# Optimization experiments

Measured on AMD Instinct MI355X. Metric: run time of the kernel, lower is better.

Reference implementation:

```python
import jax, jax.numpy as jnp
import numpy as np


def _l2n(v, axis):
    # torch F.normalize: x / max(||x||, eps)
    return v / jnp.maximum(jnp.linalg.norm(v, axis=axis, keepdims=True), 1e-12)


def setup_inputs() -> dict:
    key = jax.random.key(0)
    ks = jax.random.split(key, 10)
    B, C, H, W = 32, 1536, 32, 32
    m, l, g, hid = 64, 128, 256, 512
    s = 0.02
    f32 = jnp.float32
    return {
        "x": jax.random.normal(ks[0], (B, C, H, W), f32),
        "t": jax.random.normal(ks[1], (B, C), f32),
        "Wc1": jax.random.normal(ks[2], (hid, C), f32) * s, "bc1": jnp.zeros(hid, f32),
        "Wc2": jax.random.normal(ks[3], (l, hid), f32) * s, "bc2": jnp.zeros(l, f32),
        "Ws1": jax.random.normal(ks[4], (hid, C), f32) * s, "bs1": jnp.zeros(hid, f32),
        "Ws2": jax.random.normal(ks[5], (m, hid), f32) * s, "bs2": jnp.zeros(m, f32),
        "Wt1": jax.random.normal(ks[6], (hid, C), f32) * s, "bt1": jnp.zeros(hid, f32),
        "Wt2": jax.random.normal(ks[7], (g, hid), f32) * s, "bt2": jnp.zeros(g, f32),
        "dust_bin": jnp.asarray(1.0, f32),
        "burst_a": jnp.asarray(1.0, f32),
        "burst_b": jnp.asarray(0.0, f32),
        "burst_p": jnp.asarray(1.0, f32),
    }


def reference(x, t, Wc1, bc1, Wc2, bc2, Ws1, bs1, Ws2, bs2,
              Wt1, bt1, Wt2, bt2, dust_bin, burst_a, burst_b, burst_p):
    B, C, H, W = x.shape
    n = H * W
    dt = x.dtype
    xf = x.reshape(B, C, n)

    # 1x1 conv stacks == per-pixel linear layers over channel dim
    h = jax.nn.relu(jnp.einsum('oc,bcn->bon', Wc1, xf) + bc1[None, :, None])
    f = jnp.einsum('oc,bcn->bon', Wc2, h) + bc2[None, :, None]          # [B,l,n]
    hs = jax.nn.relu(jnp.einsum('oc,bcn->bon', Ws1, xf) + bs1[None, :, None])
    p = jnp.einsum('oc,bcn->bon', Ws2, hs) + bs2[None, :, None]         # [B,m,n]

    # token MLP
    tk = jax.nn.relu(t @ Wt1.T + bt1) @ Wt2.T + bt2                     # [B,g]

    # log-space optimal transport (Sinkhorn, 3 iters)
    m = p.shape[1]
    norm = -jnp.log(jnp.asarray(m + n, dt))
    log_mu = jnp.concatenate([jnp.full((m,), norm, dt),
                              (jnp.log(jnp.asarray(n, dt)) + norm)[None]])  # [m+1]
    log_nu = jnp.full((n,), norm, dt)                                      # [n]
    Z = jnp.concatenate([p, jnp.broadcast_to(dust_bin, (B, 1, n))], axis=1)  # [B,m+1,n]
    u = jnp.zeros((B, m + 1), dt)
    v = jnp.zeros((B, n), dt)
    for _ in range(3):
        u = log_mu[None] - jax.nn.logsumexp(Z + v[:, None, :], axis=2)
        v = log_nu[None] - jax.nn.logsumexp(Z + u[:, :, None], axis=1)
    P = jnp.exp(Z + u[:, :, None] + v[:, None, :] - norm)[:, :-1, :]    # [B,m,n]

    # burst reweighting
    fn = _l2n(f, 1)
    sim = jnp.einsum('bln,blk->bnk', fn, fn)                            # [B,n,n]
    bw_sum = jax.nn.sigmoid(burst_a * sim + burst_b).sum(axis=-1)       # [B,n]
    P = P / (bw_sum ** burst_p)[:, None, :]

    # VLAD-style soft aggregation: (f[:,l,None,n] * P[:,None,m,n]).sum(-1)
    agg = jnp.einsum('bln,bmn->blm', f, P)                              # [B,l,m]
    agg = _l2n(agg, 1).reshape(B, -1)                                   # [B,l*m]

    out = jnp.concatenate([_l2n(tk, -1), agg], axis=-1)
    return _l2n(out, -1)
```

## Files before the change

kernel.cpp:

```cpp
#include <hip/hip_runtime.h>
#include <math.h>

#define B_   32
#define C_   1536
#define N_   1024
#define HID_ 512
#define L_   128
#define M_   64
#define G_   256

typedef unsigned short u16;
typedef unsigned int   u32;
typedef short bf16x8 __attribute__((ext_vector_type(8)));
typedef float f32x4  __attribute__((ext_vector_type(4)));

__device__ __forceinline__ u16 f2bf(float v) {
    u32 u = __float_as_uint(v);
    return (u16)((u + 0x7fffu + ((u >> 16) & 1u)) >> 16);
}
__device__ __forceinline__ float bf2f(u16 b) { return __uint_as_float(((u32)b) << 16); }
__device__ __forceinline__ float bflo(u32 u) { return __uint_as_float(u << 16); }
__device__ __forceinline__ float bfhi(u32 u) { return __uint_as_float(u & 0xffff0000u); }

__device__ __forceinline__ void gload16(const u16* g, u16* l) {
    __builtin_amdgcn_global_load_lds(
        (const __attribute__((address_space(1))) void*)g,
        (__attribute__((address_space(3))) void*)l, 16, 0, 0);
}

__global__ __launch_bounds__(256)
void k_split(const float* __restrict__ src, u16* __restrict__ h, u16* __restrict__ l, int n4)
{
    const int i = blockIdx.x * 256 + threadIdx.x;
    if (i >= n4) return;
    const float4 v = ((const float4*)src)[i];
    const u16 h0 = f2bf(v.x), h1 = f2bf(v.y), h2 = f2bf(v.z), h3 = f2bf(v.w);
    *(uint2*)&h[(size_t)i * 4] =
        make_uint2((u32)h0 | ((u32)h1 << 16), (u32)h2 | ((u32)h3 << 16));
    const u16 l0 = f2bf(v.x - bf2f(h0)), l1 = f2bf(v.y - bf2f(h1));
    const u16 l2 = f2bf(v.z - bf2f(h2)), l3 = f2bf(v.w - bf2f(h3));
    *(uint2*)&l[(size_t)i * 4] =
        make_uint2((u32)l0 | ((u32)l1 << 16), (u32)l2 | ((u32)l3 << 16));
}

template<int THIRD>
__global__ __launch_bounds__(256)
void k_prep_xt(const float* __restrict__ x, u16* __restrict__ xTh, u16* __restrict__ xTl)
{
    __shared__ float T[64][65];
    const int tid = threadIdx.x;
    const int j0 = blockIdx.x * 64, c0 = blockIdx.y * 64, b = blockIdx.z;
    const int row = tid >> 2, cq = (tid & 3) * 16;
    const float* src = x + ((size_t)b * C_ + c0 + row) * N_ + j0 + cq;
    *(float4*)&T[row][cq + 0]  = *(const float4*)(src + 0);
    *(float4*)&T[row][cq + 4]  = *(const float4*)(src + 4);
    *(float4*)&T[row][cq + 8]  = *(const float4*)(src + 8);
    *(float4*)&T[row][cq + 12] = *(const float4*)(src + 12);
    __syncthreads();
    u32 ph[8], pl[8];
    #pragma unroll
    for (int i2 = 0; i2 < 8; ++i2) {
        const float f0 = T[cq + i2 * 2][row], f1 = T[cq + i2 * 2 + 1][row];
        const u16 h0 = f2bf(f0), h1 = f2bf(f1);
        ph[i2] = (u32)h0 | ((u32)h1 << 16);
        if (THIRD) {
            const u16 l0 = f2bf(f0 - bf2f(h0)), l1 = f2bf(f1 - bf2f(h1));
            pl[i2] = (u32)l0 | ((u32)l1 << 16);
        }
    }
    u16* dh = xTh + ((size_t)b * N_ + j0 + row) * C_ + c0 + cq;
    *(uint4*)(dh + 0) = make_uint4(ph[0], ph[1], ph[2], ph[3]);
    *(uint4*)(dh + 8) = make_uint4(ph[4], ph[5], ph[6], ph[7]);
    if (THIRD) {
        u16* dl = xTl + ((size_t)b * N_ + j0 + row) * C_ + c0 + cq;
        *(uint4*)(dl + 0) = make_uint4(pl[0], pl[1], pl[2], pl[3]);
        *(uint4*)(dl + 8) = make_uint4(pl[4], pl[5], pl[6], pl[7]);
    }
}

template<int THIRD>
__global__ __launch_bounds__(256)
void k_conv1_mfma(const u16* __restrict__ A1h, const u16* __restrict__ A1l,
                  const u16* __restrict__ xTh, const u16* __restrict__ xTl,
                  const float* __restrict__ bc1, const float* __restrict__ bs1,
                  u16* __restrict__ H1Th, u16* __restrict__ H1Tl)
{
    __shared__ u16 sm[17408];
    const int tid = threadIdx.x;
    const int j0 = blockIdx.x * 128, o0 = blockIdx.y * 128, b = blockIdx.z;

    const int r0 = tid & 127, kb0 = tid >> 7;
    const size_t aOff0 = (size_t)(o0 + r0) * C_ + kb0 * 8;
    const size_t aOff1 = aOff0 + 16;
    const size_t bOff0 = ((size_t)b * N_ + j0 + r0) * C_ + kb0 * 8;
    const size_t bOff1 = bOff0 + 16;

    const int w = tid >> 6, lane = tid & 63;
    const int wr = w >> 1, wc = w & 1, q = lane >> 4, r16 = lane & 15;
    const int aBase = (q * 128 + wr * 64 + r16) * 8;
    const int bBase = (q * 128 + wc * 64 + r16) * 8;

    f32x4 acc[4][4] = {};
    for (int k0 = 0; k0 < C_; k0 += 32) {
        __syncthreads();
        gload16(A1h + aOff0 + k0, &sm[tid * 8]);
        gload16(A1h + aOff1 + k0, &sm[(tid + 256) * 8]);
        gload16(A1l + aOff0 + k0, &sm[4096 + tid * 8]);
        gload16(A1l + aOff1 + k0, &sm[4096 + (tid + 256) * 8]);
        gload16(xTh + bOff0 + k0, &sm[8192 + tid * 8]);
        gload16(xTh + bOff1 + k0, &sm[8192 + (tid + 256) * 8]);
        if (THIRD) {
            gload16(xTl + bOff0 + k0, &sm[12288 + tid * 8]);
            gload16(xTl + bOff1 + k0, &sm[12288 + (tid + 256) * 8]);
        }
        __syncthreads();
        bf16x8 ah[4], al[4], bh[4], bl[4];
        #pragma unroll
        for (int m = 0; m < 4; ++m) {
            ah[m] = *(const bf16x8*)&sm[aBase + m * 128];
            al[m] = *(const bf16x8*)&sm[4096 + aBase + m * 128];
        }
        #pragma unroll
        for (int n = 0; n < 4; ++n) {
            bh[n] = *(const bf16x8*)&sm[8192 + bBase + n * 128];
            if (THIRD) bl[n] = *(const bf16x8*)&sm[12288 + bBase + n * 128];
        }
        #pragma unroll
        for (int m = 0; m < 4; ++m)
            #pragma unroll
            for (int n = 0; n < 4; ++n) {
                acc[m][n] = __builtin_amdgcn_mfma_f32_16x16x32_bf16(ah[m], bh[n], acc[m][n], 0, 0, 0);
                acc[m][n] = __builtin_amdgcn_mfma_f32_16x16x32_bf16(al[m], bh[n], acc[m][n], 0, 0, 0);
                if (THIRD)
                    acc[m][n] = __builtin_amdgcn_mfma_f32_16x16x32_bf16(ah[m], bl[n], acc[m][n], 0, 0, 0);
            }
    }
    const float* bb = (o0 < HID_) ? (bc1 + o0) : (bs1 + (o0 - HID_));
    const int oB = wr * 64 + q * 4;
    const int jB = wc * 64 + r16;
    #pragma unroll
    for (int pass = 0; pass < 2; ++pass) {
        __syncthreads();
        #pragma unroll
        for (int m = 0; m < 4; ++m)
            #pragma unroll
            for (int n = 0; n < 4; ++n) {
                u16 h4[4];
                #pragma unroll
                for (int r = 0; r < 4; ++r) {
                    const float v = fmaxf(acc[m][n][r] + bb[oB + m * 16 + r], 0.f);
                    const u16 hi = f2bf(v);
                    h4[r] = pass ? f2bf(v - bf2f(hi)) : hi;
                }
                *(uint2*)&sm[(jB + n * 16) * 136 + oB + m * 16] =
                    make_uint2((u32)h4[0] | ((u32)h4[1] << 16), (u32)h4[2] | ((u32)h4[3] << 16));
            }
        __syncthreads();
        u16* dst = pass ? H1Tl : H1Th;
        #pragma unroll
        for (int p = 0; p < 8; ++p) {
            const int j = p * 16 + (tid >> 4);
            const int col = (tid & 15) * 8;
            *(uint4*)&dst[((size_t)b * N_ + j0 + j) * 1024 + o0 + col] =
                *(const uint4*)&sm[j * 136 + col];
        }
    }
}

__global__ __launch_bounds__(256)
void k_conv2_mfma(const u16* __restrict__ A2h, const u16* __restrict__ A2l,
                  const u16* __restrict__ H1Th, const u16* __restrict__ H1Tl,
                  const float* __restrict__ bc2, const float* __restrict__ bs2,
                  float* __restrict__ ff, u16* __restrict__ fTh, float* __restrict__ pbuf)
{
    __shared__ u16 sm[12288];
    const int tid = threadIdx.x;
    const int j0 = blockIdx.x * 128, mt = blockIdx.y, b = blockIdx.z;
    const int koff = (mt == 2) ? HID_ : 0;

    const int rA = tid & 63, kbA = tid >> 6;
    const size_t aOff = (size_t)(mt * 64 + rA) * HID_ + kbA * 8;
    const int rB = tid & 127, kbB = tid >> 7;
    const size_t bOff  = ((size_t)b * N_ + j0 + rB) * 1024 + koff + kbB * 8;
    const size_t bOff1 = bOff + 16;

    const int w = tid >> 6, lane = tid & 63;
    const int wr = w >> 1, wc = w & 1, q = lane >> 4, r16 = lane & 15;

    f32x4 acc[2][4] = {};
    for (int k0 = 0; k0 < HID_; k0 += 32) {
        __syncthreads();
        gload16(A2h + aOff + k0, &sm[tid * 8]);
        gload16(A2l + aOff + k0, &sm[2048 + tid * 8]);
        gload16(H1Th + bOff + k0,  &sm[4096 + tid * 8]);
        gload16(H1Th + bOff1 + k0, &sm[4096 + (tid + 256) * 8]);
        gload16(H1Tl + bOff + k0,  &sm[8192 + tid * 8]);
        gload16(H1Tl + bOff1 + k0, &sm[8192 + (tid + 256) * 8]);
        __syncthreads();
        bf16x8 ah[2], al[2], bh[4], bl[4];
        #pragma unroll
        for (int m = 0; m < 2; ++m) {
            const int idx = (q * 64 + wr * 32 + m * 16 + r16) * 8;
            ah[m] = *(const bf16x8*)&sm[idx];
            al[m] = *(const bf16x8*)&sm[2048 + idx];
        }
        #pragma unroll
        for (int n = 0; n < 4; ++n) {
            const int idx = (q * 128 + wc * 64 + n * 16 + r16) * 8;
            bh[n] = *(const bf16x8*)&sm[4096 + idx];
            bl[n] = *(const bf16x8*)&sm[8192 + idx];
        }
        #pragma unroll
        for (int m = 0; m < 2; ++m)
            #pragma unroll
            for (int n = 0; n < 4; ++n) {
                acc[m][n] = __builtin_amdgcn_mfma_f32_16x16x32_bf16(ah[m], bh[n], acc[m][n], 0, 0, 0);
                acc[m][n] = __builtin_amdgcn_mfma_f32_16x16x32_bf16(al[m], bh[n], acc[m][n], 0, 0, 0);
                acc[m][n] = __builtin_amdgcn_mfma_f32_16x16x32_bf16(ah[m], bl[n], acc[m][n], 0, 0, 0);
            }
    }
    const float* bb = (mt == 0) ? bc2 : (mt == 1 ? bc2 + 64 : bs2);
    #pragma unroll
    for (int m = 0; m < 2; ++m) {
        const int lB = wr * 32 + m * 16 + q * 4;
        #pragma unroll
        for (int n = 0; n < 4; ++n) {
            const int jl = wc * 64 + n * 16 + r16;
            float v[4];
            #pragma unroll
            for (int r = 0; r < 4; ++r) v[r] = acc[m][n][r] + bb[lB + r];
            if (mt < 2) {
                #pragma unroll
                for (int r = 0; r < 4; ++r)
                    ff[((size_t)b * L_ + mt * 64 + lB + r) * N_ + j0 + jl] = v[r];
                *(uint2*)&fTh[((size_t)b * N_ + j0 + jl) * L_ + mt * 64 + lB] =
                    make_uint2((u32)f2bf(v[0]) | ((u32)f2bf(v[1]) << 16),
                               (u32)f2bf(v[2]) | ((u32)f2bf(v[3]) << 16));
            } else {
                #pragma unroll
                for (int r = 0; r < 4; ++r)
                    pbuf[((size_t)b * M_ + lB + r) * N_ + j0 + jl] = v[r];
            }
        }
    }
}

__global__ __launch_bounds__(256)
void k_fn(const u16* __restrict__ fTh, u16* __restrict__ fnT)
{
    const int tid = threadIdx.x;
    const int row = blockIdx.x * 32 + (tid >> 3);
    const int l8 = tid & 7;
    const u16* src = fTh + (size_t)row * L_ + l8 * 16;
    const uint4 va = *(const uint4*)src;
    const uint4 vb = *(const uint4*)(src + 8);
    float f[16];
    f[0]=bflo(va.x); f[1]=bfhi(va.x); f[2]=bflo(va.y); f[3]=bfhi(va.y);
    f[4]=bflo(va.z); f[5]=bfhi(va.z); f[6]=bflo(va.w); f[7]=bfhi(va.w);
    f[8]=bflo(vb.x); f[9]=bfhi(vb.x); f[10]=bflo(vb.y); f[11]=bfhi(vb.y);
    f[12]=bflo(vb.z); f[13]=bfhi(vb.z); f[14]=bflo(vb.w); f[15]=bfhi(vb.w);
    float ss = 0.f;
    #pragma unroll
    for (int i = 0; i < 16; ++i) ss = fmaf(f[i], f[i], ss);
    ss += __shfl_xor(ss, 1); ss += __shfl_xor(ss, 2); ss += __shfl_xor(ss, 4);
    const float inv = 1.f / fmaxf(sqrtf(ss), 1e-12f);
    u32 p[8];
    #pragma unroll
    for (int i2 = 0; i2 < 8; ++i2)
        p[i2] = (u32)f2bf(f[i2*2] * inv) | ((u32)f2bf(f[i2*2+1] * inv) << 16);
    u16* dst = fnT + (size_t)row * L_ + l8 * 16;
    *(uint4*)(dst + 0) = make_uint4(p[0], p[1], p[2], p[3]);
    *(uint4*)(dst + 8) = make_uint4(p[4], p[5], p[6], p[7]);
}

__global__ __launch_bounds__(256)
void k_zero(float* __restrict__ p, int n)
{
    const int i = blockIdx.x * 256 + threadIdx.x;
    if (i < n) p[i] = 0.f;
}

__global__ __launch_bounds__(256)
void k_burst_mfma(const u16* __restrict__ fnT, const float* __restrict__ pa,
                  const float* __restrict__ pbv, float* __restrict__ bw)
{
    __shared__ u16 sm[8192];
    const int tid = threadIdx.x;
    const int j0 = blockIdx.x * 128, k0t = blockIdx.y * 128, b = blockIdx.z;
    const float aa = *pa, bcst = *pbv;

    const int rB = tid & 127, kbB = tid >> 7;
    const size_t aOff  = ((size_t)b * N_ + j0 + rB) * L_ + kbB * 8;
    const size_t aOff1 = aOff + 16;
    const size_t bOff  = ((size_t)b * N_ + k0t + rB) * L_ + kbB * 8;
    const size_t bOff1 = bOff + 16;

    const int w = tid >> 6, lane = tid & 63;
    const int wr = w >> 1, wc = w & 1, q = lane >> 4, r16 = lane & 15;
    const int aBase = (q * 128 + wr * 64 + r16) * 8;
    const int bBase = (q * 128 + wc * 64 + r16) * 8;

    f32x4 acc[4][4] = {};
    for (int k0 = 0; k0 < L_; k0 += 32) {
        __syncthreads();
        gload16(fnT + aOff + k0,  &sm[tid * 8]);
        gload16(fnT + aOff1 + k0, &sm[(tid + 256) * 8]);
        gload16(fnT + bOff + k0,  &sm[4096 + tid * 8]);
        gload16(fnT + bOff1 + k0, &sm[4096 + (tid + 256) * 8]);
        __syncthreads();
        bf16x8 a[4], bv[4];
        #pragma unroll
        for (int m = 0; m < 4; ++m) a[m]  = *(const bf16x8*)&sm[aBase + m * 128];
        #pragma unroll
        for (int n = 0; n < 4; ++n) bv[n] = *(const bf16x8*)&sm[4096 + bBase + n * 128];
        #pragma unroll
        for (int m = 0; m < 4; ++m)
            #pragma unroll
            for (int n = 0; n < 4; ++n)
                acc[m][n] = __builtin_amdgcn_mfma_f32_16x16x32_bf16(a[m], bv[n], acc[m][n], 0, 0, 0);
    }
    #pragma unroll
    for (int m = 0; m < 4; ++m)
        #pragma unroll
        for (int r = 0; r < 4; ++r) {
            float s = 0.f;
            #pragma unroll
            for (int n = 0; n < 4; ++n)
                s += 1.f / (1.f + __expf(-(fmaf(aa, acc[m][n][r], bcst))));
            s += __shfl_xor(s, 1); s += __shfl_xor(s, 2);
            s += __shfl_xor(s, 4); s += __shfl_xor(s, 8);
            if (r16 == 0)
                atomicAdd(&bw[b * N_ + j0 + wr * 64 + m * 16 + q * 4 + r], s);
        }
}

__global__ __launch_bounds__(256)
void k_tok1(const float* __restrict__ t, const float* __restrict__ W,
            const float* __restrict__ bias, float* __restrict__ outv)
{
    const int b = blockIdx.y;
    const int o = blockIdx.x * 8 + (threadIdx.x >> 5);
    const int lane = threadIdx.x & 31;
    const float* tb = t + (size_t)b * C_;
    const float* wv = W + (size_t)o * C_;
    float s = 0.f;
    for (int c = lane; c < C_; c += 32) s = fmaf(wv[c], tb[c], s);
    for (int off = 16; off; off >>= 1) s += __shfl_down(s, off, 32);
    if (lane == 0) outv[b * HID_ + o] = fmaxf(s + bias[o], 0.f);
}

__global__ __launch_bounds__(256)
void k_tok2(const float* __restrict__ h, const float* __restrict__ W,
            const float* __restrict__ bias, float* __restrict__ outv)
{
    const int b = blockIdx.y;
    const int o = blockIdx.x * 8 + (threadIdx.x >> 5);
    const int lane = threadIdx.x & 31;
    const float* hb = h + (size_t)b * HID_;
    const float* wv = W + (size_t)o * HID_;
    float s = 0.f;
    for (int c = lane; c < HID_; c += 32) s = fmaf(wv[c], hb[c], s);
    for (int off = 16; off; off >>= 1) s += __shfl_down(s, off, 32);
    if (lane == 0) outv[b * G_ + o] = s + bias[o];
}

__global__ __launch_bounds__(1024)
void k_sinkhorn(const float* __restrict__ pbuf, const float* __restrict__ dustp,
                float* __restrict__ Pbuf)
{
    const int b = blockIdx.x;
    const int tid = threadIdx.x;
    const float dust = *dustp;
    const float* Zb = pbuf + (size_t)b * M_ * N_;
    float* Pb = Pbuf + (size_t)b * M_ * N_;
    __shared__ float v_s[N_];
    __shared__ float u_s[M_ + 1];
    const float normc = -logf(1088.0f);
    const float lmu_dust = logf(1024.0f) + normc;

    v_s[tid] = 0.f;
    __syncthreads();
    const int wv = tid >> 6, lane = tid & 63;

    for (int it = 0; it < 3; ++it) {
        for (int i = wv; i < 65; i += 16) {
            float zz[16];
            #pragma unroll
            for (int qq = 0; qq < 16; ++qq) {
                const int j = lane + (qq << 6);
                const float z = (i < 64) ? Zb[(size_t)i * N_ + j] : dust;
                zz[qq] = z + v_s[j];
            }
            float mx = zz[0];
            #pragma unroll
            for (int qq = 1; qq < 16; ++qq) mx = fmaxf(mx, zz[qq]);
            #pragma unroll
            for (int off = 32; off; off >>= 1) mx = fmaxf(mx, __shfl_xor(mx, off));
            float s = 0.f;
            #pragma unroll
            for (int qq = 0; qq < 16; ++qq) s += __expf(zz[qq] - mx);
            #pragma unroll
            for (int off = 32; off; off >>= 1) s += __shfl_xor(s, off);
            if (lane == 0)
                u_s[i] = ((i < 64) ? normc : lmu_dust) - (mx + __logf(s));
        }
        __syncthreads();
        {
            float mx = -INFINITY, s = 0.f;
            for (int i = 0; i < 64; ++i) {
                const float z = Zb[(size_t)i * N_ + tid] + u_s[i];
                const float nm = fmaxf(mx, z);
                s = s * __expf(mx - nm) + __expf(z - nm);
                mx = nm;
            }
            { const float z = dust + u_s[64];
              const float nm = fmaxf(mx, z);
              s = s * __expf(mx - nm) + __expf(z - nm);
              mx = nm; }
            v_s[tid] = normc - (mx + __logf(s));
        }
        __syncthreads();
    }
    const float vvv = v_s[tid];
    for (int i = 0; i < 64; ++i)
        Pb[(size_t)i * N_ + tid] =
            __expf(Zb[(size_t)i * N_ + tid] + u_s[i] + vvv - normc);
}

__global__ __launch_bounds__(256)
void k_agg(const float* __restrict__ fbuf, const float* __restrict__ Pbuf,
           const float* __restrict__ bw, const float* __restrict__ bp,
           float* __restrict__ agg)
{
    const int b = blockIdx.x;
    const int l0 = blockIdx.y * 32;
    const float pw = *bp;
    const float* fb = fbuf + ((size_t)b * L_ + l0) * N_;
    const float* Pb = Pbuf + (size_t)b * M_ * N_;
    const float* bwb = bw + b * N_;
    __shared__ float Fs[32][65];
    __shared__ float Ps[64][65];
    const int tid = threadIdx.x;
    const int tx = tid & 15, ty = tid >> 4;
    float acc[2][4];
    #pragma unroll
    for (int i = 0; i < 2; ++i)
        #pragma unroll
        for (int qq = 0; qq < 4; ++qq) acc[i][qq] = 0.f;

    for (int j0 = 0; j0 < N_; j0 += 64) {
        __syncthreads();
        for (int idx = tid; idx < 32 * 64; idx += 256) {
            const int li = idx >> 6, jj = idx & 63;
            Fs[li][jj] = fb[(size_t)li * N_ + j0 + jj];
        }
        for (int idx = tid; idx < 64 * 64; idx += 256) {
            const int mi = idx >> 6, jj = idx & 63;
            const float iwv = __expf(-pw * __logf(bwb[j0 + jj]));
            Ps[mi][jj] = Pb[(size_t)mi * N_ + j0 + jj] * iwv;
        }
        __syncthreads();
        for (int jj = 0; jj < 64; ++jj) {
            const float a0 = Fs[ty * 2 + 0][jj];
            const float a1 = Fs[ty * 2 + 1][jj];
            #pragma unroll
            for (int qq = 0; qq < 4; ++qq) {
                const float bq = Ps[tx * 4 + qq][jj];
                acc[0][qq] = fmaf(a0, bq, acc[0][qq]);
                acc[1][qq] = fmaf(a1, bq, acc[1][qq]);
            }
        }
    }
    #pragma unroll
    for (int i = 0; i < 2; ++i)
        #pragma unroll
        for (int qq = 0; qq < 4; ++qq)
            agg[((size_t)b * L_ + l0 + ty * 2 + i) * M_ + tx * 4 + qq] = acc[i][qq];
}

__global__ __launch_bounds__(256)
void k_final(const float* __restrict__ tk, const float* __restrict__ agg,
             float* __restrict__ out)
{
    const int b = blockIdx.x;
    const int tid = threadIdx.x;
    const float* ab = agg + (size_t)b * L_ * M_;
    __shared__ float red[256];
    __shared__ float colred[4][64];
    __shared__ float sa[64];
    __shared__ float bcast[2];

    const float tv = tk[b * G_ + tid];
    red[tid] = tv * tv;
    __syncthreads();
    for (int s = 128; s > 0; s >>= 1) { if (tid < s) red[tid] += red[tid + s]; __syncthreads(); }
    if (tid == 0) bcast[0] = 1.f / fmaxf(sqrtf(red[0]), 1e-12f);
    __syncthreads();
    const float tkn = tv * bcast[0];

    const int mi = tid & 63, part = tid >> 6;
    float cs = 0.f;
    for (int li = part; li < L_; li += 4) { const float v = ab[li * M_ + mi]; cs = fmaf(v, v, cs); }
    colred[part][mi] = cs;
    __syncthreads();
    if (tid < 64)
        sa[tid] = 1.f / fmaxf(sqrtf(colred[0][tid] + colred[1][tid] +
                                    colred[2][tid] + colred[3][tid]), 1e-12f);
    __syncthreads();

    float tot = tkn * tkn;
    for (int idx = tid; idx < L_ * M_; idx += 256) {
        const float v = ab[idx] * sa[idx & 63];
        tot = fmaf(v, v, tot);
    }
    __syncthreads();
    red[tid] = tot;
    __syncthreads();
    for (int s = 128; s > 0; s >>= 1) { if (tid < s) red[tid] += red[tid + s]; __syncthreads(); }
    if (tid == 0) bcast[1] = 1.f / fmaxf(sqrtf(red[0]), 1e-12f);
    __syncthreads();
    const float invT = bcast[1];

    float* ob = out + (size_t)b * (G_ + L_ * M_);
    ob[tid] = tkn * invT;
    for (int idx = tid; idx < L_ * M_; idx += 256)
        ob[G_ + idx] = ab[idx] * sa[idx & 63] * invT;
}

extern "C" void kernel_launch(void* const* d_in, const int* in_sizes, int n_in,
                              void* d_out, int out_size, void* d_ws, size_t ws_size,
                              hipStream_t stream)
{
    const float* x    = (const float*)d_in[0];
    const float* t    = (const float*)d_in[1];
    const float* Wc1  = (const float*)d_in[2];
    const float* bc1  = (const float*)d_in[3];
    const float* Wc2  = (const float*)d_in[4];
    const float* bc2  = (const float*)d_in[5];
    const float* Ws1  = (const float*)d_in[6];
    const float* bs1  = (const float*)d_in[7];
    const float* Ws2  = (const float*)d_in[8];
    const float* bs2  = (const float*)d_in[9];
    const float* Wt1  = (const float*)d_in[10];
    const float* bt1  = (const float*)d_in[11];
    const float* Wt2  = (const float*)d_in[12];
    const float* bt2  = (const float*)d_in[13];
    const float* dust = (const float*)d_in[14];
    const float* ba   = (const float*)d_in[15];
    const float* bbv  = (const float*)d_in[16];
    const float* bp   = (const float*)d_in[17];

    char* ws = (char*)d_ws;
    u16* A1h  = (u16*)(ws + 0);
    u16* A1l  = (u16*)(ws + 3145728);
    u16* A2h  = (u16*)(ws + 6291456);
    u16* A2l  = (u16*)(ws + 6488064);
    u16* H1Th = (u16*)(ws + 6684672);
    u16* H1Tl = (u16*)(ws + 73793536);
    float* tkb = (float*)(ws + 140902400);
    float* htb = (float*)(ws + 140935168);
    float* bw  = (float*)(ws + 141000704);
    const size_t base0 = 141131776;
    u16*   xTh  = (u16*)(ws + base0);
    float* pb   = (float*)(ws + base0);
    float* Pb   = (float*)(ws + base0 + 8388608);
    u16*   fTh  = (u16*)(ws + base0 + 16777216);
    u16*   fnT  = (u16*)(ws + base0 + 25165824);
    float* ff   = (float*)(ws + base0 + 33554432);
    float* aggb = (float*)(ws + base0 + 50331648);
    const size_t NEED3 = base0 + 2ull * 100663296ull;
    u16* xTl = (u16*)(ws + base0 + 100663296);
    const bool third = (ws_size >= NEED3);
    if (!third) xTl = xTh;

    k_split<<<768, 256, 0, stream>>>(Wc1, A1h, A1l, 512 * C_ / 4);
    k_split<<<768, 256, 0, stream>>>(Ws1, A1h + (size_t)512 * C_, A1l + (size_t)512 * C_, 512 * C_ / 4);
    k_split<<<64, 256, 0, stream>>>(Wc2, A2h, A2l, 128 * HID_ / 4);
    k_split<<<32, 256, 0, stream>>>(Ws2, A2h + (size_t)128 * HID_, A2l + (size_t)128 * HID_, 64 * HID_ / 4);
    if (third) k_prep_xt<1><<<dim3(16, 24, B_), 256, 0, stream>>>(x, xTh, xTl);
    else       k_prep_xt<0><<<dim3(16, 24, B_), 256, 0, stream>>>(x, xTh, xTl);

    if (third) k_conv1_mfma<1><<<dim3(8, 8, B_), 256, 0, stream>>>(A1h, A1l, xTh, xTl, bc1, bs1, H1Th, H1Tl);
    else       k_conv1_mfma<0><<<dim3(8, 8, B_), 256, 0, stream>>>(A1h, A1l, xTh, xTl, bc1, bs1, H1Th, H1Tl);
    k_conv2_mfma<<<dim3(8, 3, B_), 256, 0, stream>>>(A2h, A2l, H1Th, H1Tl, bc2, bs2, ff, fTh, pb);

    k_tok1<<<dim3(64, B_), 256, 0, stream>>>(t, Wt1, bt1, htb);
    k_tok2<<<dim3(32, B_), 256, 0, stream>>>(htb, Wt2, bt2, tkb);

    k_sinkhorn<<<dim3(B_), 1024, 0, stream>>>(pb, dust, Pb);

    k_fn<<<1024, 256, 0, stream>>>(fTh, fnT);
    k_zero<<<128, 256, 0, stream>>>(bw, B_ * N_);
    k_burst_mfma<<<dim3(8, 8, B_), 256, 0, stream>>>(fnT, ba, bbv, bw);

    k_agg<<<dim3(B_, 4), 256, 0, stream>>>(ff, Pb, bw, bp, aggb);
    k_final<<<dim3(B_), 256, 0, stream>>>(tkb, aggb, (float*)d_out);
}
```

Measured before the change: 1.102 ms.

## Rewrite conv1 GEMM with 256x256 tiles, double-buffered LDS prefetch and setprio

```diff
diff --git a/kernel.cpp b/kernel.cpp
--- a/kernel.cpp
+++ b/kernel.cpp
@@ -79,92 +79,133 @@
 }
 
 template<int THIRD>
-__global__ __launch_bounds__(256)
-void k_conv1_mfma(const u16* __restrict__ A1h, const u16* __restrict__ A1l,
-                  const u16* __restrict__ xTh, const u16* __restrict__ xTl,
-                  const float* __restrict__ bc1, const float* __restrict__ bs1,
-                  u16* __restrict__ H1Th, u16* __restrict__ H1Tl)
-{
-    __shared__ u16 sm[17408];
-    const int tid = threadIdx.x;
-    const int j0 = blockIdx.x * 128, o0 = blockIdx.y * 128, b = blockIdx.z;
-
-    const int r0 = tid & 127, kb0 = tid >> 7;
-    const size_t aOff0 = (size_t)(o0 + r0) * C_ + kb0 * 8;
-    const size_t aOff1 = aOff0 + 16;
-    const size_t bOff0 = ((size_t)b * N_ + j0 + r0) * C_ + kb0 * 8;
-    const size_t bOff1 = bOff0 + 16;
+__global__ __launch_bounds__(512, 2)
+void k_conv1_v3(const u16* __restrict__ A1h, const u16* __restrict__ A1l,
+                const u16* __restrict__ xTh, const u16* __restrict__ xTl,
+                const float* __restrict__ bc1, const float* __restrict__ bs1,
+                u16* __restrict__ H1Th, u16* __restrict__ H1Tl)
+{
+    __shared__ u16 sm[65536];
+    const int tid = threadIdx.x;
+    const int j0 = blockIdx.x * 256, o0 = blockIdx.y * 256, b = blockIdx.z;
+
+    const int r256 = tid & 255, qb = tid >> 8;
+    const size_t aG = (size_t)(o0 + r256) * C_ + qb * 8;
+    const size_t bG = ((size_t)b * N_ + j0 + r256) * C_ + qb * 8;
+    const int s0 = tid * 8;
 
     const int w = tid >> 6, lane = tid & 63;
-    const int wr = w >> 1, wc = w & 1, q = lane >> 4, r16 = lane & 15;
-    const int aBase = (q * 128 + wr * 64 + r16) * 8;
-    const int bBase = (q * 128 + wc * 64 + r16) * 8;
-
-    f32x4 acc[4][4] = {};
-    for (int k0 = 0; k0 < C_; k0 += 32) {
-        __syncthreads();
-        gload16(A1h + aOff0 + k0, &sm[tid * 8]);
-        gload16(A1h + aOff1 + k0, &sm[(tid + 256) * 8]);
-        gload16(A1l + aOff0 + k0, &sm[4096 + tid * 8]);
-        gload16(A1l + aOff1 + k0, &sm[4096 + (tid + 256) * 8]);
-        gload16(xTh + bOff0 + k0, &sm[8192 + tid * 8]);
-        gload16(xTh + bOff1 + k0, &sm[8192 + (tid + 256) * 8]);
-        if (THIRD) {
-            gload16(xTl + bOff0 + k0, &sm[12288 + tid * 8]);
-            gload16(xTl + bOff1 + k0, &sm[12288 + (tid + 256) * 8]);
-        }
-        __syncthreads();
-        bf16x8 ah[4], al[4], bh[4], bl[4];
-        #pragma unroll
-        for (int m = 0; m < 4; ++m) {
-            ah[m] = *(const bf16x8*)&sm[aBase + m * 128];
-            al[m] = *(const bf16x8*)&sm[4096 + aBase + m * 128];
-        }
-        #pragma unroll
-        for (int n = 0; n < 4; ++n) {
-            bh[n] = *(const bf16x8*)&sm[8192 + bBase + n * 128];
-            if (THIRD) bl[n] = *(const bf16x8*)&sm[12288 + bBase + n * 128];
-        }
-        #pragma unroll
-        for (int m = 0; m < 4; ++m)
-            #pragma unroll
-            for (int n = 0; n < 4; ++n) {
-                acc[m][n] = __builtin_amdgcn_mfma_f32_16x16x32_bf16(ah[m], bh[n], acc[m][n], 0, 0, 0);
-                acc[m][n] = __builtin_amdgcn_mfma_f32_16x16x32_bf16(al[m], bh[n], acc[m][n], 0, 0, 0);
+    const int wr = w >> 2, wc = w & 3, q = lane >> 4, r16 = lane & 15;
+    const int aB = (q * 256 + wr * 128 + r16) * 8;
+    const int bB = 16384 + (q * 256 + wc * 64 + r16) * 8;
+
+    f32x4 acc[8][4] = {};
+
+    gload16(A1h + aG,      &sm[s0]);
+    gload16(A1h + aG + 16, &sm[4096 + s0]);
+    gload16(A1l + aG,      &sm[8192 + s0]);
+    gload16(A1l + aG + 16, &sm[8192 + 4096 + s0]);
+    gload16(xTh + bG,      &sm[16384 + s0]);
+    gload16(xTh + bG + 16, &sm[16384 + 4096 + s0]);
+    if (THIRD) {
+        gload16(xTl + bG,      &sm[24576 + s0]);
+        gload16(xTl + bG + 16, &sm[24576 + 4096 + s0]);
+    }
+    __syncthreads();
+
+    for (int t = 0; t < 48; ++t) {
+        const int cb = (t & 1) << 15;
+        const int nb = cb ^ 32768;
+        const size_t kn = (size_t)(t + 1) * 32;
+        const bool pf = (t < 47);
+        #pragma unroll
+        for (int p = 0; p < 4; ++p) {
+            const int mh = p >> 1, nh = p & 1;
+            bf16x8 ah[4], al[4], bh[2], bl[2];
+            #pragma unroll
+            for (int i = 0; i < 4; ++i) {
+                ah[i] = *(const bf16x8*)&sm[cb + aB + (mh * 4 + i) * 128];
+                al[i] = *(const bf16x8*)&sm[cb + 8192 + aB + (mh * 4 + i) * 128];
+            }
+            #pragma unroll
+            for (int nn = 0; nn < 2; ++nn) {
+                bh[nn] = *(const bf16x8*)&sm[cb + bB + (nh * 2 + nn) * 128];
                 if (THIRD)
-                    acc[m][n] = __builtin_amdgcn_mfma_f32_16x16x32_bf16(ah[m], bl[n], acc[m][n], 0, 0, 0);
-            }
-    }
+                    bl[nn] = *(const bf16x8*)&sm[cb + 8192 + bB + (nh * 2 + nn) * 128];
+            }
+            if (p == 0 && pf) {
+                gload16(A1h + aG + kn,      &sm[nb + s0]);
+                gload16(A1h + aG + kn + 16, &sm[nb + 4096 + s0]);
+                gload16(A1l + aG + kn,      &sm[nb + 8192 + s0]);
+                gload16(A1l + aG + kn + 16, &sm[nb + 8192 + 4096 + s0]);
+            }
+            if (p == 1 && pf) {
+                gload16(xTh + bG + kn,      &sm[nb + 16384 + s0]);
+                gload16(xTh + bG + kn + 16, &sm[nb + 16384 + 4096 + s0]);
+                if (THIRD) {
+                    gload16(xTl + bG + kn,      &sm[nb + 24576 + s0]);
+                    gload16(xTl + bG + kn + 16, &sm[nb + 24576 + 4096 + s0]);
+                }
+            }
+            __builtin_amdgcn_s_barrier();
+            __builtin_amdgcn_s_setprio(1);
+            #pragma unroll
+            for (int i = 0; i < 4; ++i)
+                #pragma unroll
+                for (int nn = 0; nn < 2; ++nn) {
+                    const int mi = mh * 4 + i, ni = nh * 2 + nn;
+                    acc[mi][ni] = __builtin_amdgcn_mfma_f32_16x16x32_bf16(ah[i], bh[nn], acc[mi][ni], 0, 0, 0);
+                    acc[mi][ni] = __builtin_amdgcn_mfma_f32_16x16x32_bf16(al[i], bh[nn], acc[mi][ni], 0, 0, 0);
+                    if (THIRD)
+                        acc[mi][ni] = __builtin_amdgcn_mfma_f32_16x16x32_bf16(ah[i], bl[nn], acc[mi][ni], 0, 0, 0);
+                }
+            __builtin_amdgcn_s_setprio(0);
+            __builtin_amdgcn_s_barrier();
+        }
+        __syncthreads();
+    }
+
     const float* bb = (o0 < HID_) ? (bc1 + o0) : (bs1 + (o0 - HID_));
-    const int oB = wr * 64 + q * 4;
-    const int jB = wc * 64 + r16;
-    #pragma unroll
-    for (int pass = 0; pass < 2; ++pass) {
-        __syncthreads();
-        #pragma unroll
-        for (int m = 0; m < 4; ++m)
-            #pragma unroll
-            for (int n = 0; n < 4; ++n) {
-                u16 h4[4];
+    #pragma unroll
+    for (int m = 0; m < 8; ++m)
+        #pragma unroll
+        for (int r = 0; r < 4; ++r) {
+            const float bv = bb[wr * 128 + m * 16 + q * 4 + r];
+            #pragma unroll
+            for (int n = 0; n < 4; ++n)
+                acc[m][n][r] = fmaxf(acc[m][n][r] + bv, 0.f);
+        }
+
+    const int jq = wc >> 1;
+    const int jl0 = (wc & 1) * 64;
+    for (int pass = 0; pass < 2; ++pass)
+        for (int jh = 0; jh < 2; ++jh) {
+            __syncthreads();
+            if (jq == jh) {
                 #pragma unroll
-                for (int r = 0; r < 4; ++r) {
-                    const float v = fmaxf(acc[m][n][r] + bb[oB + m * 16 + r], 0.f);
-                    const u16 hi = f2bf(v);
-                    h4[r] = pass ? f2bf(v - bf2f(hi)) : hi;
-                }
-                *(uint2*)&sm[(jB + n * 16) * 136 + oB + m * 16] =
-                    make_uint2((u32)h4[0] | ((u32)h4[1] << 16), (u32)h4[2] | ((u32)h4[3] << 16));
-            }
-        __syncthreads();
-        u16* dst = pass ? H1Tl : H1Th;
-        #pragma unroll
-        for (int p = 0; p < 8; ++p) {
-            const int j = p * 16 + (tid >> 4);
-            const int col = (tid & 15) * 8;
-            *(uint4*)&dst[((size_t)b * N_ + j0 + j) * 1024 + o0 + col] =
-                *(const uint4*)&sm[j * 136 + col];
-        }
-    }
+                for (int m = 0; m < 8; ++m)
+                    #pragma unroll
+                    for (int n = 0; n < 4; ++n) {
+                        u16 o4[4];
+                        #pragma unroll
+                        for (int r = 0; r < 4; ++r) {
+                            const float v = acc[m][n][r];
+                            const u16 hi = f2bf(v);
+                            o4[r] = pass ? f2bf(v - bf2f(hi)) : hi;
+                        }
+                        *(uint2*)&sm[(jl0 + n * 16 + r16) * 264 + wr * 128 + m * 16 + q * 4] =
+                            make_uint2((u32)o4[0] | ((u32)o4[1] << 16),
+                                       (u32)o4[2] | ((u32)o4[3] << 16));
+                    }
+            }
+            __syncthreads();
+            const int jr = tid >> 2, ck = (tid & 3) * 64;
+            u16* dst = (pass ? H1Tl : H1Th) +
+                       ((size_t)b * N_ + j0 + jh * 128 + jr) * 1024 + o0 + ck;
+            #pragma unroll
+            for (int u = 0; u < 8; ++u)
+                *(uint4*)(dst + u * 8) = *(const uint4*)&sm[jr * 264 + ck + u * 8];
+        }
 }
 
 __global__ __launch_bounds__(256)
@@ -580,8 +621,8 @@
     if (third) k_prep_xt<1><<<dim3(16, 24, B_), 256, 0, stream>>>(x, xTh, xTl);
     else       k_prep_xt<0><<<dim3(16, 24, B_), 256, 0, stream>>>(x, xTh, xTl);
 
-    if (third) k_conv1_mfma<1><<<dim3(8, 8, B_), 256, 0, stream>>>(A1h, A1l, xTh, xTl, bc1, bs1, H1Th, H1Tl);
-    else       k_conv1_mfma<0><<<dim3(8, 8, B_), 256, 0, stream>>>(A1h, A1l, xTh, xTl, bc1, bs1, H1Th, H1Tl);
+    if (third) k_conv1_v3<1><<<dim3(4, 4, B_), 512, 0, stream>>>(A1h, A1l, xTh, xTl, bc1, bs1, H1Th, H1Tl);
+    else       k_conv1_v3<0><<<dim3(4, 4, B_), 512, 0, stream>>>(A1h, A1l, xTh, xTl, bc1, bs1, H1Th, H1Tl);
     k_conv2_mfma<<<dim3(8, 3, B_), 256, 0, stream>>>(A2h, A2l, H1Th, H1Tl, bc2, bs2, ff, fTh, pb);
 
     k_tok1<<<dim3(64, B_), 256, 0, stream>>>(t, Wt1, bt1, htb);
```

After: 1.265 ms. +14.7%, slower.
